# Optimization experiments

Measured on AMD Instinct MI355X. Metric: run time of the kernel, lower is better.

Reference implementation:

```python
import jax, jax.numpy as jnp
import numpy as np

N_NODES = 50000
N_EDGES = 800000
F_IN = 64
HIDDEN = 64
N_CLASSES = 8
NUM_GRAPHS = 500


def setup_inputs() -> dict:
    key = jax.random.key(0)
    ks = jax.random.split(key, 12)
    x = jax.random.normal(ks[0], (N_NODES, F_IN), dtype=jnp.float32)
    edge_index = jax.random.randint(ks[1], (2, N_EDGES), 0, N_NODES, dtype=jnp.int64)
    batch = jnp.sort(jax.random.randint(ks[2], (N_NODES,), 0, NUM_GRAPHS, dtype=jnp.int64))
    def glorot(k, fan_in, fan_out):
        s = (6.0 / (fan_in + fan_out)) ** 0.5
        return jax.random.uniform(k, (fan_in, fan_out), jnp.float32, -s, s)
    return {
        "x": x,
        "edge_index": edge_index,
        "batch": batch,
        "W1": glorot(ks[3], F_IN, HIDDEN), "b1": jnp.zeros((HIDDEN,), jnp.float32),
        "W2": glorot(ks[4], HIDDEN, HIDDEN), "b2": jnp.zeros((HIDDEN,), jnp.float32),
        "W3": glorot(ks[5], HIDDEN, HIDDEN), "b3": jnp.zeros((HIDDEN,), jnp.float32),
        "Wl": glorot(ks[6], HIDDEN, N_CLASSES), "bl": jnp.zeros((N_CLASSES,), jnp.float32),
    }


def _gcn_conv(x, row, col, norm, W, b, n):
    # GCNConv: linear transform, gather source nodes, scale by sym-norm, scatter-add to targets.
    xw = x @ W                                  # [N, H]
    msg = xw[row] * norm[:, None]               # [E+N, H]
    out = jax.ops.segment_sum(msg, col, num_segments=n)
    return out + b


def reference(x, edge_index, batch, W1, b1, W2, b2, W3, b3, Wl, bl):
    n = x.shape[0]
    loop = jnp.arange(n, dtype=edge_index.dtype)
    row = jnp.concatenate([edge_index[0], loop])  # source nodes (+ self loops)
    col = jnp.concatenate([edge_index[1], loop])  # target nodes (+ self loops)
    deg = jax.ops.segment_sum(jnp.ones_like(col, dtype=x.dtype), col, num_segments=n)
    dinv = jnp.where(deg > 0, jax.lax.rsqrt(deg), 0.0)
    norm = dinv[row] * dinv[col]                # symmetric normalization per edge

    h = jax.nn.relu(_gcn_conv(x, row, col, norm, W1, b1, n))
    h = jax.nn.relu(_gcn_conv(h, row, col, norm, W2, b2, n))
    h = _gcn_conv(h, row, col, norm, W3, b3, n)

    # global mean pool over graphs
    sums = jax.ops.segment_sum(h, batch, num_segments=NUM_GRAPHS)
    cnts = jax.ops.segment_sum(jnp.ones((n,), x.dtype), batch, num_segments=NUM_GRAPHS)
    embed = sums / jnp.maximum(cnts, 1.0)[:, None]

    # dropout p=0.5 is identity in eval mode
    return embed @ Wl + bl
```

## Files before the change

### kernel.cpp

```cpp
#include <hip/hip_runtime.h>
#include <hip/hip_bf16.h>
#include <hip/hip_fp16.h>

#define HID      64
#define N_CLS    8
#define N_GRAPHS 500
#define PAD      64
#define BW       128
#define NB       391
#define CHUNK    4096
#define CAP_BLK  48

__global__ __launch_bounds__(1024) void k_bin(
        const int* __restrict__ row, const int* __restrict__ col, int E,
        unsigned int* __restrict__ ebuf, unsigned short* __restrict__ cnt_tbl,
        int* __restrict__ bcnt) {
    __shared__ int cur[NB];
    int t = threadIdx.x, bi = blockIdx.x;
    if (bi == 0 && t < 512) bcnt[t] = 0;
    for (int i = t; i < NB; i += 1024) cur[i] = 0;
    __syncthreads();
    int e = bi * CHUNK + t * 4;
    if (e < E) {
        int4 c4 = *reinterpret_cast<const int4*>(col + e);
        int4 r4 = *reinterpret_cast<const int4*>(row + e);
        int b0 = c4.x >> 7, b1 = c4.y >> 7, b2 = c4.z >> 7, b3 = c4.w >> 7;
        int s0 = atomicAdd(&cur[b0], 1);
        int s1 = atomicAdd(&cur[b1], 1);
        int s2 = atomicAdd(&cur[b2], 1);
        int s3 = atomicAdd(&cur[b3], 1);
        size_t base = (size_t)bi * NB;
        if (s0 < CAP_BLK) ebuf[(base + b0) * CAP_BLK + s0] = ((unsigned)(c4.x & 127) << 16) | (unsigned)r4.x;
        if (s1 < CAP_BLK) ebuf[(base + b1) * CAP_BLK + s1] = ((unsigned)(c4.y & 127) << 16) | (unsigned)r4.y;
        if (s2 < CAP_BLK) ebuf[(base + b2) * CAP_BLK + s2] = ((unsigned)(c4.z & 127) << 16) | (unsigned)r4.z;
        if (s3 < CAP_BLK) ebuf[(base + b3) * CAP_BLK + s3] = ((unsigned)(c4.w & 127) << 16) | (unsigned)r4.w;
    }
    __syncthreads();
    for (int i = t; i < NB; i += 1024)
        cnt_tbl[(size_t)bi * NB + i] = (unsigned short)min(cur[i], CAP_BLK);
}

__global__ __launch_bounds__(512) void k_fill(const unsigned int* __restrict__ ebuf,
                                              const unsigned short* __restrict__ cnt_tbl,
                                              int nEb,
                                              unsigned short* __restrict__ adj,
                                              int* __restrict__ cnt,
                                              float* __restrict__ dinv, int N,
                                              const int* __restrict__ batch,
                                              int* __restrict__ bcnt) {
    int t = threadIdx.x;
    if ((int)blockIdx.x >= NB) {
        int i = (blockIdx.x - NB) * 512 + t;
        if (i < N) atomicAdd(&bcnt[batch[i]], 1);
        return;
    }
    int b = blockIdx.x;
    __shared__ int pfx[256];
    __shared__ int lcnt[BW];
    if (t < BW) lcnt[t] = 0;
    if (t < 256) pfx[t] = (t < nEb) ? (int)cnt_tbl[(size_t)t * NB + b] : 0;
    __syncthreads();
    #pragma unroll
    for (int off = 1; off < 256; off <<= 1) {
        int v = (t < 256 && t >= off) ? pfx[t - off] : 0;
        __syncthreads();
        if (t < 256) pfx[t] += v;
        __syncthreads();
    }
    int m = pfx[nEb - 1];
    for (int g = t; g < m; g += 512) {
        int lo = 0, hi = nEb - 1;
        while (lo < hi) {
            int mid = (lo + hi) >> 1;
            if (pfx[mid] > g) hi = mid; else lo = mid + 1;
        }
        int bi = lo;
        int sl = g - (bi ? pfx[bi - 1] : 0);
        unsigned u = ebuf[((size_t)bi * NB + b) * CAP_BLK + sl];
        int cl = u >> 16;
        int r  = u & 0xFFFF;
        int p = atomicAdd(&lcnt[cl], 1);
        if (p < PAD) adj[((size_t)(b * BW + cl)) * PAD + p] = (unsigned short)r;
    }
    __syncthreads();
    int node = b * BW + t;
    if (t < BW && node < N) {
        int n = lcnt[t];
        cnt[node] = n;
        dinv[node] = rsqrtf((float)n + 1.0f);
    }
}

__global__ __launch_bounds__(256) void k_gemm64(const float* __restrict__ H,
                                                const float* __restrict__ W,
                                                const float* __restrict__ dinv,
                                                __half* __restrict__ O, int N) {
    __shared__ float Ws[64 * 64];
    int tid = threadIdx.x;
    #pragma unroll
    for (int i = tid; i < 64 * 64; i += 256) Ws[i] = W[i];
    __syncthreads();
    int c = tid & 63;
    float w[64];
    #pragma unroll
    for (int k = 0; k < 64; ++k) w[k] = Ws[k * 64 + c];

    int rbase = blockIdx.x * 32 + (tid >> 6) * 8;
    #pragma unroll 1
    for (int it = 0; it < 8; it += 2) {
        int r0 = rbase + it;
        if (r0 >= N) break;
        int r0u = __builtin_amdgcn_readfirstlane(r0);
        int has1 = (r0u + 1 < N);
        const float* __restrict__ h0 = H + (size_t)r0u * HID;
        const float* __restrict__ h1 = H + (size_t)(has1 ? r0u + 1 : r0u) * HID;
        float a0 = 0.f, a1 = 0.f, a2 = 0.f, a3 = 0.f;
        float b0 = 0.f, b1 = 0.f, b2 = 0.f, b3 = 0.f;
        #pragma unroll
        for (int k = 0; k < 64; k += 4) {
            a0 = fmaf(h0[k],     w[k],     a0);
            b0 = fmaf(h1[k],     w[k],     b0);
            a1 = fmaf(h0[k + 1], w[k + 1], a1);
            b1 = fmaf(h1[k + 1], w[k + 1], b1);
            a2 = fmaf(h0[k + 2], w[k + 2], a2);
            b2 = fmaf(h1[k + 2], w[k + 2], b2);
            a3 = fmaf(h0[k + 3], w[k + 3], a3);
            b3 = fmaf(h1[k + 3], w[k + 3], b3);
        }
        O[(size_t)r0u * HID + c] = __float2half(((a0 + a1) + (a2 + a3)) * dinv[r0u]);
        if (has1)
            O[(size_t)(r0u + 1) * HID + c] =
                __float2half(((b0 + b1) + (b2 + b3)) * dinv[r0u + 1]);
    }
}

__global__ __launch_bounds__(256) void k_gather(const unsigned short* __restrict__ adj,
                                                const int* __restrict__ cnt,
                                                const float* __restrict__ dinv,
                                                const __half* __restrict__ xh,
                                                const float* __restrict__ b,
                                                float* __restrict__ out,
                                                int N, int do_relu) {
    int node = blockIdx.x * 4 + (threadIdx.x >> 6);
    if (node >= N) return;
    int lane = threadIdx.x & 63;
    int o = lane >> 3, j = lane & 7;
    size_t s = (size_t)node * PAD;
    int n = min(cnt[node], PAD);
    float dv = dinv[node];
    int r_all = adj[s + lane];

    float a[8] = {0.f, 0.f, 0.f, 0.f, 0.f, 0.f, 0.f, 0.f};
    for (int base = 0; base < n; base += 16) {
        int i1 = base + o;
        int i2 = base + 8 + o;
        int r1 = __shfl(r_all, i1, 64);
        int r2 = __shfl(r_all, i2, 64);
        if (i1 < n) {
            uint4 u = *reinterpret_cast<const uint4*>(xh + (size_t)r1 * HID + j * 8);
            float2 f0 = __half22float2(*reinterpret_cast<__half2*>(&u.x));
            float2 f1 = __half22float2(*reinterpret_cast<__half2*>(&u.y));
            float2 f2 = __half22float2(*reinterpret_cast<__half2*>(&u.z));
            float2 f3 = __half22float2(*reinterpret_cast<__half2*>(&u.w));
            a[0] += f0.x; a[1] += f0.y; a[2] += f1.x; a[3] += f1.y;
            a[4] += f2.x; a[5] += f2.y; a[6] += f3.x; a[7] += f3.y;
        }
        if (i2 < n) {
            uint4 u = *reinterpret_cast<const uint4*>(xh + (size_t)r2 * HID + j * 8);
            float2 f0 = __half22float2(*reinterpret_cast<__half2*>(&u.x));
            float2 f1 = __half22float2(*reinterpret_cast<__half2*>(&u.y));
            float2 f2 = __half22float2(*reinterpret_cast<__half2*>(&u.z));
            float2 f3 = __half22float2(*reinterpret_cast<__half2*>(&u.w));
            a[0] += f0.x; a[1] += f0.y; a[2] += f1.x; a[3] += f1.y;
            a[4] += f2.x; a[5] += f2.y; a[6] += f3.x; a[7] += f3.y;
        }
    }
    if (o == 0) {
        uint4 u = *reinterpret_cast<const uint4*>(xh + (size_t)node * HID + j * 8);
        float2 f0 = __half22float2(*reinterpret_cast<__half2*>(&u.x));
        float2 f1 = __half22float2(*reinterpret_cast<__half2*>(&u.y));
        float2 f2 = __half22float2(*reinterpret_cast<__half2*>(&u.z));
        float2 f3 = __half22float2(*reinterpret_cast<__half2*>(&u.w));
        a[0] += f0.x; a[1] += f0.y; a[2] += f1.x; a[3] += f1.y;
        a[4] += f2.x; a[5] += f2.y; a[6] += f3.x; a[7] += f3.y;
    }
    #pragma unroll
    for (int k = 0; k < 8; ++k) {
        a[k] += __shfl_xor(a[k], 8, 64);
        a[k] += __shfl_xor(a[k], 16, 64);
        a[k] += __shfl_xor(a[k], 32, 64);
    }
    if (o == 0) {
        const float4 b0 = *reinterpret_cast<const float4*>(b + j * 8);
        const float4 b1 = *reinterpret_cast<const float4*>(b + j * 8 + 4);
        float4 o0, o1;
        o0.x = a[0] * dv + b0.x; o0.y = a[1] * dv + b0.y;
        o0.z = a[2] * dv + b0.z; o0.w = a[3] * dv + b0.w;
        o1.x = a[4] * dv + b1.x; o1.y = a[5] * dv + b1.y;
        o1.z = a[6] * dv + b1.z; o1.w = a[7] * dv + b1.w;
        if (do_relu) {
            o0.x = fmaxf(o0.x, 0.f); o0.y = fmaxf(o0.y, 0.f);
            o0.z = fmaxf(o0.z, 0.f); o0.w = fmaxf(o0.w, 0.f);
            o1.x = fmaxf(o1.x, 0.f); o1.y = fmaxf(o1.y, 0.f);
            o1.z = fmaxf(o1.z, 0.f); o1.w = fmaxf(o1.w, 0.f);
        }
        *reinterpret_cast<float4*>(out + (size_t)node * HID + j * 8)     = o0;
        *reinterpret_cast<float4*>(out + (size_t)node * HID + j * 8 + 4) = o1;
    }
}

__global__ __launch_bounds__(256) void k_fgh2(const unsigned short* __restrict__ adj,
                                              const int* __restrict__ cnt,
                                              const float* __restrict__ dinv,
                                              const __half* __restrict__ xh,
                                              const float* __restrict__ b,
                                              const float* __restrict__ Wl,
                                              float* __restrict__ y,
                                              int N) {
    int node = blockIdx.x * 4 + (threadIdx.x >> 6);
    if (node >= N) return;
    int lane = threadIdx.x & 63;
    int o = lane >> 3, j = lane & 7;
    size_t s = (size_t)node * PAD;
    int n = min(cnt[node], PAD);
    float dv = dinv[node];
    int r_all = adj[s + lane];

    float a[8] = {0.f, 0.f, 0.f, 0.f, 0.f, 0.f, 0.f, 0.f};
    for (int base = 0; base < n; base += 16) {
        int i1 = base + o;
        int i2 = base + 8 + o;
        int r1 = __shfl(r_all, i1, 64);
        int r2 = __shfl(r_all, i2, 64);
        if (i1 < n) {
            uint4 u = *reinterpret_cast<const uint4*>(xh + (size_t)r1 * HID + j * 8);
            float2 f0 = __half22float2(*reinterpret_cast<__half2*>(&u.x));
            float2 f1 = __half22float2(*reinterpret_cast<__half2*>(&u.y));
            float2 f2 = __half22float2(*reinterpret_cast<__half2*>(&u.z));
            float2 f3 = __half22float2(*reinterpret_cast<__half2*>(&u.w));
            a[0] += f0.x; a[1] += f0.y; a[2] += f1.x; a[3] += f1.y;
            a[4] += f2.x; a[5] += f2.y; a[6] += f3.x; a[7] += f3.y;
        }
        if (i2 < n) {
            uint4 u = *reinterpret_cast<const uint4*>(xh + (size_t)r2 * HID + j * 8);
            float2 f0 = __half22float2(*reinterpret_cast<__half2*>(&u.x));
            float2 f1 = __half22float2(*reinterpret_cast<__half2*>(&u.y));
            float2 f2 = __half22float2(*reinterpret_cast<__half2*>(&u.z));
            float2 f3 = __half22float2(*reinterpret_cast<__half2*>(&u.w));
            a[0] += f0.x; a[1] += f0.y; a[2] += f1.x; a[3] += f1.y;
            a[4] += f2.x; a[5] += f2.y; a[6] += f3.x; a[7] += f3.y;
        }
    }
    if (o == 0) {
        uint4 u = *reinterpret_cast<const uint4*>(xh + (size_t)node * HID + j * 8);
        float2 f0 = __half22float2(*reinterpret_cast<__half2*>(&u.x));
        float2 f1 = __half22float2(*reinterpret_cast<__half2*>(&u.y));
        float2 f2 = __half22float2(*reinterpret_cast<__half2*>(&u.z));
        float2 f3 = __half22float2(*reinterpret_cast<__half2*>(&u.w));
        a[0] += f0.x; a[1] += f0.y; a[2] += f1.x; a[3] += f1.y;
        a[4] += f2.x; a[5] += f2.y; a[6] += f3.x; a[7] += f3.y;
    }
    #pragma unroll
    for (int k = 0; k < 8; ++k) {
        a[k] += __shfl_xor(a[k], 8, 64);
        a[k] += __shfl_xor(a[k], 16, 64);
        a[k] += __shfl_xor(a[k], 32, 64);
    }
    const float4 bv0 = *reinterpret_cast<const float4*>(b + j * 8);
    const float4 bv1 = *reinterpret_cast<const float4*>(b + j * 8 + 4);
    float h[8];
    h[0] = fmaf(a[0], dv, bv0.x); h[1] = fmaf(a[1], dv, bv0.y);
    h[2] = fmaf(a[2], dv, bv0.z); h[3] = fmaf(a[3], dv, bv0.w);
    h[4] = fmaf(a[4], dv, bv1.x); h[5] = fmaf(a[5], dv, bv1.y);
    h[6] = fmaf(a[6], dv, bv1.z); h[7] = fmaf(a[7], dv, bv1.w);
    float p = 0.f;
    #pragma unroll
    for (int m = 0; m < 8; ++m)
        p = fmaf(h[m], Wl[(j * 8 + m) * N_CLS + o], p);
    p += __shfl_xor(p, 1, 64);
    p += __shfl_xor(p, 2, 64);
    p += __shfl_xor(p, 4, 64);
    if (j == 0) y[(size_t)node * N_CLS + o] = p;
}

__global__ __launch_bounds__(256) void k_pmean8(const float* __restrict__ y,
                                                const int* __restrict__ bcnt,
                                                const float* __restrict__ bl,
                                                float* __restrict__ out) {
    int g = blockIdx.x;
    int t = threadIdx.x;
    __shared__ int ssum[256];
    int part = 0;
    for (int k = t; k < g; k += 256) part += bcnt[k];
    ssum[t] = part;
    __syncthreads();
    for (int s2 = 128; s2 > 0; s2 >>= 1) {
        if (t < s2) ssum[t] += ssum[t + s2];
        __syncthreads();
    }
    int s = ssum[0];
    int n = bcnt[g];
    int c = t & 7, idx = t >> 3;
    float acc = 0.f;
    for (int i = s + idx; i < s + n; i += 32) acc += y[(size_t)i * N_CLS + c];
    __shared__ float lds[256];
    lds[t] = acc;
    __syncthreads();
    for (int s2 = 16; s2 > 0; s2 >>= 1) {
        if (idx < s2) lds[t] += lds[t + s2 * 8];
        __syncthreads();
    }
    if (t < N_CLS)
        out[(size_t)g * N_CLS + t] = lds[t] / fmaxf((float)n, 1.0f) + bl[t];
}

extern "C" void kernel_launch(void* const* d_in, const int* in_sizes, int n_in,
                              void* d_out, int out_size, void* d_ws, size_t ws_size,
                              hipStream_t stream) {
    const float* x     = (const float*)d_in[0];
    const int*   ei    = (const int*)d_in[1];
    const int*   batch = (const int*)d_in[2];
    const float* W1    = (const float*)d_in[3];
    const float* b1    = (const float*)d_in[4];
    const float* W2    = (const float*)d_in[5];
    const float* b2    = (const float*)d_in[6];
    const float* W3    = (const float*)d_in[7];
    const float* b3    = (const float*)d_in[8];
    const float* Wl    = (const float*)d_in[9];
    const float* bl    = (const float*)d_in[10];
    float* out = (float*)d_out;

    const int N = in_sizes[0] / HID;
    const int E = in_sizes[1] / 2;
    const int* row = ei;
    const int* col = ei + E;

    const int nEb = (E + CHUNK - 1) / CHUNK;

    char* wsb = (char*)d_ws;
    int*   bcnt = (int*)wsb;
    int*   cnt  = bcnt + 512;
    float* dinv = (float*)(cnt + 50048);
    unsigned short* cnt_tbl = (unsigned short*)(dinv + 50048);
    unsigned int*   ebuf    = (unsigned int*)((int*)cnt_tbl + 40000);
    unsigned short* adj     = (unsigned short*)(ebuf + (size_t)nEb * NB * CAP_BLK);
    __half* bufH = (__half*)(adj + (size_t)50048 * PAD);
    float*  bufB = (float*)(bufH + (size_t)50048 * HID);
    float*  ybuf = bufB + (size_t)50048 * HID;

    const int T = 256;
    const int nF2   = (N + 511) / 512;
    const int gGemm = (N + 31) / 32;
    const int gGath = (N + 3) / 4;

    k_bin <<<nEb, 1024, 0, stream>>>(row, col, E, ebuf, cnt_tbl, bcnt);
    k_fill<<<NB + nF2, 512, 0, stream>>>(ebuf, cnt_tbl, nEb, adj, cnt, dinv, N, batch, bcnt);

    k_gemm64<<<gGemm, T, 0, stream>>>(x, W1, dinv, bufH, N);
    k_gather<<<gGath, T, 0, stream>>>(adj, cnt, dinv, bufH, b1, bufB, N, 1);
    k_gemm64<<<gGemm, T, 0, stream>>>(bufB, W2, dinv, bufH, N);
    k_gather<<<gGath, T, 0, stream>>>(adj, cnt, dinv, bufH, b2, bufB, N, 1);
    k_gemm64<<<gGemm, T, 0, stream>>>(bufB, W3, dinv, bufH, N);
    k_fgh2<<<gGath, T, 0, stream>>>(adj, cnt, dinv, bufH, b3, Wl, ybuf, N);

    k_pmean8<<<N_GRAPHS, T, 0, stream>>>(ybuf, bcnt, bl, out);
}
```

Baseline: 208.8 us.

## Fuse first-layer GEMM into binning kernel and derive graph bounds by binary search

The first layer's X@W1 no longer depends on dinv, so it moves into extra blocks of the edge-binning kernel, which removes one launch and lets the GEMM overlap with binning. The source-side dinv scaling for layer 1 is applied per edge inside the gather, which costs an extra dinv load per edge. The per-graph node-count atomics and the prefix scan in the pooling kernel are replaced by binary searches on the sorted batch array. This relies on batch being sorted, and it makes the binning kernel's blocks heterogeneous in work.

```diff
diff --git a/kernel.cpp b/kernel.cpp
--- a/kernel.cpp
+++ b/kernel.cpp
@@ -11,33 +11,76 @@
 #define CHUNK    4096
 #define CAP_BLK  48
 
-__global__ __launch_bounds__(1024) void k_bin(
+__global__ __launch_bounds__(1024) void k_bin_gemm(
         const int* __restrict__ row, const int* __restrict__ col, int E,
         unsigned int* __restrict__ ebuf, unsigned short* __restrict__ cnt_tbl,
-        int* __restrict__ bcnt) {
-    __shared__ int cur[NB];
-    int t = threadIdx.x, bi = blockIdx.x;
-    if (bi == 0 && t < 512) bcnt[t] = 0;
-    for (int i = t; i < NB; i += 1024) cur[i] = 0;
+        const float* __restrict__ Hx, const float* __restrict__ W1,
+        const float* __restrict__ dinv_unused, __half* __restrict__ O, int N) {
+    __shared__ float smem[4096];
+    int t = threadIdx.x;
+    int nEb = (E + CHUNK - 1) / CHUNK;
+
+    if ((int)blockIdx.x < nEb) {
+        int* cur = (int*)smem;
+        int bi = blockIdx.x;
+        for (int i = t; i < NB; i += 1024) cur[i] = 0;
+        __syncthreads();
+        int e = bi * CHUNK + t * 4;
+        if (e < E) {
+            int4 c4 = *reinterpret_cast<const int4*>(col + e);
+            int4 r4 = *reinterpret_cast<const int4*>(row + e);
+            int b0 = c4.x >> 7, b1 = c4.y >> 7, b2 = c4.z >> 7, b3 = c4.w >> 7;
+            int s0 = atomicAdd(&cur[b0], 1);
+            int s1 = atomicAdd(&cur[b1], 1);
+            int s2 = atomicAdd(&cur[b2], 1);
+            int s3 = atomicAdd(&cur[b3], 1);
+            size_t base = (size_t)bi * NB;
+            if (s0 < CAP_BLK) ebuf[(base + b0) * CAP_BLK + s0] = ((unsigned)(c4.x & 127) << 16) | (unsigned)r4.x;
+            if (s1 < CAP_BLK) ebuf[(base + b1) * CAP_BLK + s1] = ((unsigned)(c4.y & 127) << 16) | (unsigned)r4.y;
+            if (s2 < CAP_BLK) ebuf[(base + b2) * CAP_BLK + s2] = ((unsigned)(c4.z & 127) << 16) | (unsigned)r4.z;
+            if (s3 < CAP_BLK) ebuf[(base + b3) * CAP_BLK + s3] = ((unsigned)(c4.w & 127) << 16) | (unsigned)r4.w;
+        }
+        __syncthreads();
+        for (int i = t; i < NB; i += 1024)
+            cnt_tbl[(size_t)bi * NB + i] = (unsigned short)min(cur[i], CAP_BLK);
+        return;
+    }
+    int gb = blockIdx.x - nEb;
+    float* Ws = smem;
+    #pragma unroll
+    for (int i = t; i < 64 * 64; i += 1024) Ws[i] = W1[i];
     __syncthreads();
-    int e = bi * CHUNK + t * 4;
-    if (e < E) {
-        int4 c4 = *reinterpret_cast<const int4*>(col + e);
-        int4 r4 = *reinterpret_cast<const int4*>(row + e);
-        int b0 = c4.x >> 7, b1 = c4.y >> 7, b2 = c4.z >> 7, b3 = c4.w >> 7;
-        int s0 = atomicAdd(&cur[b0], 1);
-        int s1 = atomicAdd(&cur[b1], 1);
-        int s2 = atomicAdd(&cur[b2], 1);
-        int s3 = atomicAdd(&cur[b3], 1);
-        size_t base = (size_t)bi * NB;
-        if (s0 < CAP_BLK) ebuf[(base + b0) * CAP_BLK + s0] = ((unsigned)(c4.x & 127) << 16) | (unsigned)r4.x;
-        if (s1 < CAP_BLK) ebuf[(base + b1) * CAP_BLK + s1] = ((unsigned)(c4.y & 127) << 16) | (unsigned)r4.y;
-        if (s2 < CAP_BLK) ebuf[(base + b2) * CAP_BLK + s2] = ((unsigned)(c4.z & 127) << 16) | (unsigned)r4.z;
-        if (s3 < CAP_BLK) ebuf[(base + b3) * CAP_BLK + s3] = ((unsigned)(c4.w & 127) << 16) | (unsigned)r4.w;
-    }
-    __syncthreads();
-    for (int i = t; i < NB; i += 1024)
-        cnt_tbl[(size_t)bi * NB + i] = (unsigned short)min(cur[i], CAP_BLK);
+    int c = t & 63;
+    float w[64];
+    #pragma unroll
+    for (int k = 0; k < 64; ++k) w[k] = Ws[k * 64 + c];
+
+    int rbase = gb * 128 + (t >> 6) * 8;
+    #pragma unroll 1
+    for (int it = 0; it < 8; it += 2) {
+        int r0 = rbase + it;
+        if (r0 >= N) break;
+        int r0u = __builtin_amdgcn_readfirstlane(r0);
+        int has1 = (r0u + 1 < N);
+        const float* __restrict__ h0 = Hx + (size_t)r0u * HID;
+        const float* __restrict__ h1 = Hx + (size_t)(has1 ? r0u + 1 : r0u) * HID;
+        float a0 = 0.f, a1 = 0.f, a2 = 0.f, a3 = 0.f;
+        float b0 = 0.f, b1 = 0.f, b2 = 0.f, b3 = 0.f;
+        #pragma unroll
+        for (int k = 0; k < 64; k += 4) {
+            a0 = fmaf(h0[k],     w[k],     a0);
+            b0 = fmaf(h1[k],     w[k],     b0);
+            a1 = fmaf(h0[k + 1], w[k + 1], a1);
+            b1 = fmaf(h1[k + 1], w[k + 1], b1);
+            a2 = fmaf(h0[k + 2], w[k + 2], a2);
+            b2 = fmaf(h1[k + 2], w[k + 2], b2);
+            a3 = fmaf(h0[k + 3], w[k + 3], a3);
+            b3 = fmaf(h1[k + 3], w[k + 3], b3);
+        }
+        O[(size_t)r0u * HID + c] = __float2half((a0 + a1) + (a2 + a3));
+        if (has1)
+            O[(size_t)(r0u + 1) * HID + c] = __float2half((b0 + b1) + (b2 + b3));
+    }
 }
 
 __global__ __launch_bounds__(512) void k_fill(const unsigned int* __restrict__ ebuf,
@@ -45,15 +88,8 @@
                                               int nEb,
                                               unsigned short* __restrict__ adj,
                                               int* __restrict__ cnt,
-                                              float* __restrict__ dinv, int N,
-                                              const int* __restrict__ batch,
-                                              int* __restrict__ bcnt) {
+                                              float* __restrict__ dinv, int N) {
     int t = threadIdx.x;
-    if ((int)blockIdx.x >= NB) {
-        int i = (blockIdx.x - NB) * 512 + t;
-        if (i < N) atomicAdd(&bcnt[batch[i]], 1);
-        return;
-    }
     int b = blockIdx.x;
     __shared__ int pfx[256];
     __shared__ int lcnt[BW];
@@ -140,7 +176,7 @@
                                                 const __half* __restrict__ xh,
                                                 const float* __restrict__ b,
                                                 float* __restrict__ out,
-                                                int N, int do_relu) {
+                                                int N, int do_relu, int edge_scale) {
     int node = blockIdx.x * 4 + (threadIdx.x >> 6);
     if (node >= N) return;
     int lane = threadIdx.x & 63;
@@ -157,32 +193,41 @@
         int r1 = __shfl(r_all, i1, 64);
         int r2 = __shfl(r_all, i2, 64);
         if (i1 < n) {
+            float sc = edge_scale ? dinv[r1] : 1.0f;
             uint4 u = *reinterpret_cast<const uint4*>(xh + (size_t)r1 * HID + j * 8);
             float2 f0 = __half22float2(*reinterpret_cast<__half2*>(&u.x));
             float2 f1 = __half22float2(*reinterpret_cast<__half2*>(&u.y));
             float2 f2 = __half22float2(*reinterpret_cast<__half2*>(&u.z));
             float2 f3 = __half22float2(*reinterpret_cast<__half2*>(&u.w));
-            a[0] += f0.x; a[1] += f0.y; a[2] += f1.x; a[3] += f1.y;
-            a[4] += f2.x; a[5] += f2.y; a[6] += f3.x; a[7] += f3.y;
+            a[0] = fmaf(f0.x, sc, a[0]); a[1] = fmaf(f0.y, sc, a[1]);
+            a[2] = fmaf(f1.x, sc, a[2]); a[3] = fmaf(f1.y, sc, a[3]);
+            a[4] = fmaf(f2.x, sc, a[4]); a[5] = fmaf(f2.y, sc, a[5]);
+            a[6] = fmaf(f3.x, sc, a[6]); a[7] = fmaf(f3.y, sc, a[7]);
         }
         if (i2 < n) {
+            float sc = edge_scale ? dinv[r2] : 1.0f;
             uint4 u = *reinterpret_cast<const uint4*>(xh + (size_t)r2 * HID + j * 8);
             float2 f0 = __half22float2(*reinterpret_cast<__half2*>(&u.x));
             float2 f1 = __half22float2(*reinterpret_cast<__half2*>(&u.y));
             float2 f2 = __half22float2(*reinterpret_cast<__half2*>(&u.z));
             float2 f3 = __half22float2(*reinterpret_cast<__half2*>(&u.w));
-            a[0] += f0.x; a[1] += f0.y; a[2] += f1.x; a[3] += f1.y;
-            a[4] += f2.x; a[5] += f2.y; a[6] += f3.x; a[7] += f3.y;
+            a[0] = fmaf(f0.x, sc, a[0]); a[1] = fmaf(f0.y, sc, a[1]);
+            a[2] = fmaf(f1.x, sc, a[2]); a[3] = fmaf(f1.y, sc, a[3]);
+            a[4] = fmaf(f2.x, sc, a[4]); a[5] = fmaf(f2.y, sc, a[5]);
+            a[6] = fmaf(f3.x, sc, a[6]); a[7] = fmaf(f3.y, sc, a[7]);
         }
     }
     if (o == 0) {
+        float sc = edge_scale ? dv : 1.0f;
         uint4 u = *reinterpret_cast<const uint4*>(xh + (size_t)node * HID + j * 8);
         float2 f0 = __half22float2(*reinterpret_cast<__half2*>(&u.x));
         float2 f1 = __half22float2(*reinterpret_cast<__half2*>(&u.y));
         float2 f2 = __half22float2(*reinterpret_cast<__half2*>(&u.z));
         float2 f3 = __half22float2(*reinterpret_cast<__half2*>(&u.w));
-        a[0] += f0.x; a[1] += f0.y; a[2] += f1.x; a[3] += f1.y;
-        a[4] += f2.x; a[5] += f2.y; a[6] += f3.x; a[7] += f3.y;
+        a[0] = fmaf(f0.x, sc, a[0]); a[1] = fmaf(f0.y, sc, a[1]);
+        a[2] = fmaf(f1.x, sc, a[2]); a[3] = fmaf(f1.y, sc, a[3]);
+        a[4] = fmaf(f2.x, sc, a[4]); a[5] = fmaf(f2.y, sc, a[5]);
+        a[6] = fmaf(f3.x, sc, a[6]); a[7] = fmaf(f3.y, sc, a[7]);
     }
     #pragma unroll
     for (int k = 0; k < 8; ++k) {
@@ -284,22 +329,18 @@
 }
 
 __global__ __launch_bounds__(256) void k_pmean8(const float* __restrict__ y,
-                                                const int* __restrict__ bcnt,
+                                                const int* __restrict__ batch, int N,
                                                 const float* __restrict__ bl,
                                                 float* __restrict__ out) {
     int g = blockIdx.x;
     int t = threadIdx.x;
-    __shared__ int ssum[256];
-    int part = 0;
-    for (int k = t; k < g; k += 256) part += bcnt[k];
-    ssum[t] = part;
-    __syncthreads();
-    for (int s2 = 128; s2 > 0; s2 >>= 1) {
-        if (t < s2) ssum[t] += ssum[t + s2];
-        __syncthreads();
-    }
-    int s = ssum[0];
-    int n = bcnt[g];
+    int lo = 0, hi = N;
+    while (lo < hi) { int mid = (lo + hi) >> 1; if (batch[mid] < g) lo = mid + 1; else hi = mid; }
+    int s = lo;
+    int lo2 = s, hi2 = N;
+    while (lo2 < hi2) { int mid = (lo2 + hi2) >> 1; if (batch[mid] < g + 1) lo2 = mid + 1; else hi2 = mid; }
+    int n = lo2 - s;
+
     int c = t & 7, idx = t >> 3;
     float acc = 0.f;
     for (int i = s + idx; i < s + n; i += 32) acc += y[(size_t)i * N_CLS + c];
@@ -338,8 +379,7 @@
     const int nEb = (E + CHUNK - 1) / CHUNK;
 
     char* wsb = (char*)d_ws;
-    int*   bcnt = (int*)wsb;
-    int*   cnt  = bcnt + 512;
+    int*   cnt  = (int*)wsb;
     float* dinv = (float*)(cnt + 50048);
     unsigned short* cnt_tbl = (unsigned short*)(dinv + 50048);
     unsigned int*   ebuf    = (unsigned int*)((int*)cnt_tbl + 40000);
@@ -349,19 +389,19 @@
     float*  ybuf = bufB + (size_t)50048 * HID;
 
     const int T = 256;
-    const int nF2   = (N + 511) / 512;
-    const int gGemm = (N + 31) / 32;
-    const int gGath = (N + 3) / 4;
-
-    k_bin <<<nEb, 1024, 0, stream>>>(row, col, E, ebuf, cnt_tbl, bcnt);
-    k_fill<<<NB + nF2, 512, 0, stream>>>(ebuf, cnt_tbl, nEb, adj, cnt, dinv, N, batch, bcnt);
-
-    k_gemm64<<<gGemm, T, 0, stream>>>(x, W1, dinv, bufH, N);
-    k_gather<<<gGath, T, 0, stream>>>(adj, cnt, dinv, bufH, b1, bufB, N, 1);
+    const int gGemmF = (N + 127) / 128;
+    const int gGemm  = (N + 31) / 32;
+    const int gGath  = (N + 3) / 4;
+
+    k_bin_gemm<<<nEb + gGemmF, 1024, 0, stream>>>(row, col, E, ebuf, cnt_tbl,
+                                                  x, W1, nullptr, bufH, N);
+    k_fill<<<NB, 512, 0, stream>>>(ebuf, cnt_tbl, nEb, adj, cnt, dinv, N);
+
+    k_gather<<<gGath, T, 0, stream>>>(adj, cnt, dinv, bufH, b1, bufB, N, 1, 1);
     k_gemm64<<<gGemm, T, 0, stream>>>(bufB, W2, dinv, bufH, N);
-    k_gather<<<gGath, T, 0, stream>>>(adj, cnt, dinv, bufH, b2, bufB, N, 1);
+    k_gather<<<gGath, T, 0, stream>>>(adj, cnt, dinv, bufH, b2, bufB, N, 1, 0);
     k_gemm64<<<gGemm, T, 0, stream>>>(bufB, W3, dinv, bufH, N);
     k_fgh2<<<gGath, T, 0, stream>>>(adj, cnt, dinv, bufH, b3, Wl, ybuf, N);
 
-    k_pmean8<<<N_GRAPHS, T, 0, stream>>>(ybuf, bcnt, bl, out);
-}
+    k_pmean8<<<N_GRAPHS, T, 0, stream>>>(ybuf, batch, N, bl, out);
+}
```

Measured after the change: 181.6 us. 13.0% less time.
